# Optimization experiments

Measured on AMD Instinct MI355X. Metric: run time of the kernel, lower is better.

The kernel has to match this reference:

```python
import jax, jax.numpy as jnp
import numpy as np

LOG_STD_MAX = 2.0
LOG_STD_MIN = -5.0
LN_EPS = 1e-5


def layer_norm(x, scale, bias):
    mu = jnp.mean(x, axis=-1, keepdims=True)
    var = jnp.var(x, axis=-1, keepdims=True)
    return (x - mu) * jax.lax.rsqrt(var + LN_EPS) * scale + bias


def setup_inputs() -> dict:
    key = jax.random.key(0)
    B, OBS, ACT, H, M, K = 4096, 256, 32, 512, 16, 4
    ks = jax.random.split(key, 8)
    def w(k, shape, fan_in):
        return (jax.random.normal(k, shape, jnp.float32) / np.sqrt(fan_in)).astype(jnp.float32)
    return {
        "x": jax.random.normal(ks[0], (B, OBS), jnp.float32),
        "gate_W": w(ks[1], (OBS, M), OBS),
        "gate_b": jnp.zeros((M,), jnp.float32),
        "fc1_W": w(ks[2], (OBS, H * M), OBS),
        "fc1_b": jnp.zeros((H * M,), jnp.float32),
        "norm1_scale": jnp.ones((H * M,), jnp.float32),
        "norm1_bias": jnp.zeros((H * M,), jnp.float32),
        "fc2_W": w(ks[3], (H * M, H * M), H * M),
        "fc2_b": jnp.zeros((H * M,), jnp.float32),
        "norm2_scale": jnp.ones((H * M,), jnp.float32),
        "norm2_bias": jnp.zeros((H * M,), jnp.float32),
        "mean_W": w(ks[4], (H, ACT), H),
        "mean_b": jnp.zeros((ACT,), jnp.float32),
        "logstd_W": w(ks[5], (H, ACT), H),
        "logstd_b": jnp.zeros((ACT,), jnp.float32),
        "topk": K,
    }


def reference(x, gate_W, gate_b, fc1_W, fc1_b, norm1_scale, norm1_bias,
              fc2_W, fc2_b, norm2_scale, norm2_bias,
              mean_W, mean_b, logstd_W, logstd_b, topk):
    B = x.shape[0]
    M = gate_W.shape[1]
    # gating: softmax -> topk -> renormalize -> scatter into full [B, M] scores
    gate_scores = jax.nn.softmax(x @ gate_W + gate_b, axis=-1)  # [B, M]
    topk_vals, topk_idx = jax.lax.top_k(gate_scores, topk)       # [B, K]
    topk_vals = topk_vals / jnp.sum(topk_vals, axis=-1, keepdims=True)
    scores = jnp.zeros_like(gate_scores).at[jnp.arange(B)[:, None], topk_idx].set(topk_vals)
    # trunk: Linear -> LayerNorm -> ReLU, twice
    h = jax.nn.relu(layer_norm(x @ fc1_W + fc1_b, norm1_scale, norm1_bias))
    h = jax.nn.relu(layer_norm(h @ fc2_W + fc2_b, norm2_scale, norm2_bias))
    # reshape [B, H*M] -> [B, H, M] (expert m = strided slice), weighted MEAN over experts
    h = h.reshape(B, -1, M)                                      # [B, H, M]
    mixed = jnp.einsum('bhm,bm->bh', h, scores) / M              # mean, not sum
    mean = mixed @ mean_W + mean_b
    log_std = jnp.tanh(mixed @ logstd_W + logstd_b)
    log_std = LOG_STD_MIN + 0.5 * (LOG_STD_MAX - LOG_STD_MIN) * (log_std + 1.0)
    return mean, log_std
```

## Files before the change

kernel.cpp:

```cpp
#include <hip/hip_runtime.h>
#include <hip/hip_bf16.h>

typedef unsigned int u32;
typedef unsigned short u16;
typedef __bf16 bf16x8 __attribute__((ext_vector_type(8)));
typedef float f32x4 __attribute__((ext_vector_type(4)));

__device__ __forceinline__ u16 f2b(float f) {
    __bf16 b = (__bf16)f;
    return __builtin_bit_cast(u16, b);
}
__device__ __forceinline__ float b2f(u16 v) {
    u32 x = ((u32)v) << 16;
    return __builtin_bit_cast(float, x);
}

__device__ __forceinline__ void gld_lds16(const void* g, void* l) {
    __builtin_amdgcn_global_load_lds(
        (const __attribute__((address_space(1))) u32*)(size_t)g,
        (__attribute__((address_space(3))) u32*)(u32)(size_t)l,
        16, 0, 0);
}

#define BARRIER __builtin_amdgcn_s_barrier()
#define LGKM0 asm volatile("s_waitcnt lgkmcnt(0)" ::: "memory")
#define VMC4 asm volatile("s_waitcnt vmcnt(4)" ::: "memory")
#define VMC6 asm volatile("s_waitcnt vmcnt(6)" ::: "memory")
#define VMC0 asm volatile("s_waitcnt vmcnt(0)" ::: "memory")
#define MFMA16(d, a, b) d = __builtin_amdgcn_mfma_f32_16x16x32_bf16(a, b, d, 0, 0, 0)

__global__ __launch_bounds__(256) void cast_bf16_kernel(
    const float* __restrict__ in, u16* __restrict__ out, int n4)
{
    int i = blockIdx.x * 256 + threadIdx.x;
    if (i < n4) {
        float4 f = reinterpret_cast<const float4*>(in)[i];
        u32 lo = (u32)f2b(f.x) | ((u32)f2b(f.y) << 16);
        u32 hi = (u32)f2b(f.z) | ((u32)f2b(f.w) << 16);
        uint2 o; o.x = lo; o.y = hi;
        reinterpret_cast<uint2*>(out)[i] = o;
    }
}

__global__ __launch_bounds__(256) void transpose_cast_kernel(
    const float* __restrict__ in, u16* __restrict__ out, int R, int C)
{
    __shared__ float tile[64][65];
    const int t = threadIdx.x;
    const int c0 = blockIdx.x * 64;
    const int r0 = blockIdx.y * 64;
    #pragma unroll
    for (int i = 0; i < 4; ++i) {
        int idx = t + i * 256;
        int r = idx >> 4;
        int c = (idx & 15) * 4;
        float4 f = *reinterpret_cast<const float4*>(&in[(long)(r0 + r) * C + c0 + c]);
        tile[r][c] = f.x; tile[r][c + 1] = f.y; tile[r][c + 2] = f.z; tile[r][c + 3] = f.w;
    }
    __syncthreads();
    #pragma unroll
    for (int i = 0; i < 8; ++i) {
        int idx = t + i * 256;
        int rr = idx >> 5;
        int cc = idx & 31;
        u32 p = (u32)f2b(tile[cc * 2 + 0][rr]) | ((u32)f2b(tile[cc * 2 + 1][rr]) << 16);
        *reinterpret_cast<u32*>(&out[(long)(c0 + rr) * R + r0 + cc * 2]) = p;
    }
}

__global__ __launch_bounds__(256) void gate_kernel(
    const float* __restrict__ x, const float* __restrict__ gW,
    const float* __restrict__ gb, const int* __restrict__ topk,
    float* __restrict__ scores)
{
    const int t = threadIdx.x;
    const int row = blockIdx.x * 4 + (t >> 6);
    const int l = t & 63;
    const int m = l & 15;
    const int q = l >> 4;
    const int Kk = *topk;
    const float* xr = x + (long)row * 256;
    float p = 0.f;
    #pragma unroll
    for (int k4 = 0; k4 < 16; ++k4) {
        f32x4 xv = *reinterpret_cast<const f32x4*>(xr + q * 64 + k4 * 4);
        const int kb = q * 64 + k4 * 4;
        p += xv[0] * gW[(kb + 0) * 16 + m] + xv[1] * gW[(kb + 1) * 16 + m]
           + xv[2] * gW[(kb + 2) * 16 + m] + xv[3] * gW[(kb + 3) * 16 + m];
    }
    p += __shfl_xor(p, 16);
    p += __shfl_xor(p, 32);
    float logit = p + gb[m];
    float mx = logit;
    #pragma unroll
    for (int d = 1; d < 16; d <<= 1) mx = fmaxf(mx, __shfl_xor(mx, d));
    int rank = 0;
    #pragma unroll
    for (int j = 0; j < 16; ++j) {
        float vj = __shfl(logit, (l & 48) | j);
        rank += (vj > logit) || (vj == logit && j < m);
    }
    bool sel = rank < Kk;
    float e = sel ? expf(logit - mx) : 0.f;
    float ssum = e;
    #pragma unroll
    for (int d = 1; d < 16; d <<= 1) ssum += __shfl_xor(ssum, d);
    if (q == 0) scores[row * 16 + m] = e / ssum;
}


template<int GRAN>
__device__ __forceinline__ void stage_half(
    const u16* __restrict__ src, int ld, int rowbase, int kk,
    u16* ldsregion, int h, int w, int l)
{
    #pragma unroll
    for (int j = 0; j < 2; ++j) {
        const int c = w * 2 + j;
        const int o = c * 1024 + l * 16;
        const int os = o ^ (((o >> 7) & 7) << 4);
        const int pos = o >> 7;
        const int row = ((pos / GRAN) * 2 + h) * GRAN + (pos & (GRAN - 1));
        const u16* g = src + (long)(rowbase + row) * ld + kk + ((os & 127) >> 1);
        gld_lds16(g, ldsregion + c * 512);
    }
}

__device__ __forceinline__ bf16x8 ldfrag(const u16* region, int pos, int col) {
    const int o = (pos * 128 + col * 2) ^ ((pos & 7) << 4);
    return *reinterpret_cast<const bf16x8*>(reinterpret_cast<const char*>(region) + o);
}

template<int CB>
__device__ __forceinline__ void ktile_group(
    const u16* __restrict__ A, int lda, const u16* __restrict__ BT, int ldb,
    int brow, int bcol, int kkA1, int kkR,
    int wr, int wc, int r4, int q8, int w, int l,
    u16 (&lds)[2][4][8192], f32x4 (&acc)[8][4],
    bf16x8 (&bLu)[2][2], bf16x8 (&bLf)[2][2])
{
    bf16x8 aL[4][2], aH[4][2], bH[2][2];

    #pragma unroll
    for (int m = 0; m < 4; ++m) {
        aL[m][0] = ldfrag(lds[CB][0], wr * 64 + m * 16 + r4, q8);
        aL[m][1] = ldfrag(lds[CB][0], wr * 64 + m * 16 + r4, 32 + q8);
    }
    stage_half<64>(A, lda, brow, kkA1, &lds[1 - CB][1][0], 1, w, l);
    BARRIER; LGKM0;
    __builtin_amdgcn_s_setprio(1);
    #pragma unroll
    for (int m = 0; m < 4; ++m)
        #pragma unroll
        for (int n = 0; n < 2; ++n) {
            MFMA16(acc[m][n], aL[m][0], bLu[n][0]);
            MFMA16(acc[m][n], aL[m][1], bLu[n][1]);
        }
    __builtin_amdgcn_s_setprio(0);
    BARRIER;

    #pragma unroll
    for (int n = 0; n < 2; ++n) {
        bH[n][0] = ldfrag(lds[CB][3], wc * 32 + n * 16 + r4, q8);
        bH[n][1] = ldfrag(lds[CB][3], wc * 32 + n * 16 + r4, 32 + q8);
    }
    stage_half<64>(A, lda, brow, kkR, &lds[CB][0][0], 0, w, l);
    BARRIER; LGKM0;
    __builtin_amdgcn_s_setprio(1);
    #pragma unroll
    for (int m = 0; m < 4; ++m)
        #pragma unroll
        for (int n = 0; n < 2; ++n) {
            MFMA16(acc[m][2 + n], aL[m][0], bH[n][0]);
            MFMA16(acc[m][2 + n], aL[m][1], bH[n][1]);
        }
    __builtin_amdgcn_s_setprio(0);
    BARRIER;

    #pragma unroll
    for (int m = 0; m < 4; ++m) {
        aH[m][0] = ldfrag(lds[CB][1], wr * 64 + m * 16 + r4, q8);
        aH[m][1] = ldfrag(lds[CB][1], wr * 64 + m * 16 + r4, 32 + q8);
    }
    stage_half<32>(BT, ldb, bcol, kkR, &lds[CB][2][0], 0, w, l);
    BARRIER; LGKM0;
    __builtin_amdgcn_s_setprio(1);
    #pragma unroll
    for (int m = 0; m < 4; ++m)
        #pragma unroll
        for (int n = 0; n < 2; ++n) {
            MFMA16(acc[4 + m][2 + n], aH[m][0], bH[n][0]);
            MFMA16(acc[4 + m][2 + n], aH[m][1], bH[n][1]);
        }
    __builtin_amdgcn_s_setprio(0);
    VMC4;
    BARRIER;

    #pragma unroll
    for (int n = 0; n < 2; ++n) {
        bLf[n][0] = ldfrag(lds[1 - CB][2], wc * 32 + n * 16 + r4, q8);
        bLf[n][1] = ldfrag(lds[1 - CB][2], wc * 32 + n * 16 + r4, 32 + q8);
    }
    stage_half<32>(BT, ldb, bcol, kkR, &lds[CB][3][0], 1, w, l);
    BARRIER; LGKM0;
    __builtin_amdgcn_s_setprio(1);
    #pragma unroll
    for (int m = 0; m < 4; ++m)
        #pragma unroll
        for (int n = 0; n < 2; ++n) {
            MFMA16(acc[4 + m][n], aH[m][0], bLu[n][0]);
            MFMA16(acc[4 + m][n], aH[m][1], bLu[n][1]);
        }
    __builtin_amdgcn_s_setprio(0);
    BARRIER;
}

__global__ __launch_bounds__(512, 2) void gemm256(
    const u16* __restrict__ A, int lda,
    const u16* __restrict__ BT, int ldb,
    u16* __restrict__ C, int ldc, int K)
{
    __shared__ __align__(16) u16 lds[2][4][8192];
    const int t = threadIdx.x;
    const int w = t >> 6, l = t & 63;
    const int wr = w >> 2, wc = w & 3;
    const int r4 = l & 15, q8 = (l >> 4) * 8;
    const int bid = blockIdx.y * 32 + blockIdx.x;
    const int xcd = bid & 7, within = bid >> 3;
    const int by = (xcd >> 2) * 8 + (within >> 3);
    const int bx = (xcd & 3) * 8 + (within & 7);
    const int brow = by * 256, bcol = bx * 256;
    const int NT = K >> 6;

    f32x4 acc[8][4];
    #pragma unroll
    for (int m = 0; m < 8; ++m)
        #pragma unroll
        for (int n = 0; n < 4; ++n)
            acc[m][n] = (f32x4){0.f, 0.f, 0.f, 0.f};

    stage_half<64>(A, lda, brow, 0, &lds[0][0][0], 0, w, l);
    stage_half<32>(BT, ldb, bcol, 0, &lds[0][2][0], 0, w, l);
    stage_half<32>(BT, ldb, bcol, 0, &lds[0][3][0], 1, w, l);
    stage_half<64>(A, lda, brow, 0, &lds[0][1][0], 1, w, l);
    stage_half<64>(A, lda, brow, 64, &lds[1][0][0], 0, w, l);
    stage_half<32>(BT, ldb, bcol, 64, &lds[1][2][0], 0, w, l);
    stage_half<32>(BT, ldb, bcol, 64, &lds[1][3][0], 1, w, l);
    VMC6;
    BARRIER;

    bf16x8 bl0[2][2], bl1[2][2];
    #pragma unroll
    for (int n = 0; n < 2; ++n) {
        bl0[n][0] = ldfrag(lds[0][2], wc * 32 + n * 16 + r4, q8);
        bl0[n][1] = ldfrag(lds[0][2], wc * 32 + n * 16 + r4, 32 + q8);
    }

    for (int i = 0; i < (NT >> 1); ++i) {
        const int U = 2 * i;
        int tV = U + 1;
        int tU2 = U + 2;
        int tV2 = U + 3;
        if (tU2 >= NT) tU2 -= NT;
        if (tV2 >= NT) tV2 -= NT;
        const int kkV = (tV >= NT ? tV - NT : tV) << 6;
        const int kkU2 = tU2 << 6;
        const int kkV2 = tV2 << 6;

        ktile_group<0>(A, lda, BT, ldb, brow, bcol, kkV, kkU2,
                       wr, wc, r4, q8, w, l, lds, acc, bl0, bl1);
        ktile_group<1>(A, lda, BT, ldb, brow, bcol, kkU2, kkV2,
                       wr, wc, r4, q8, w, l, lds, acc, bl1, bl0);
    }

    VMC0;

    const int crow0 = (l >> 4) * 4;
    const int ccol = l & 15;
    #pragma unroll
    for (int m = 0; m < 8; ++m) {
        #pragma unroll
        for (int n = 0; n < 4; ++n) {
            int gr = brow + wr * 128 + m * 16 + crow0;
            int gc = bcol + wc * 64 + n * 16 + ccol;
            #pragma unroll
            for (int r = 0; r < 4; ++r)
                C[(long)(gr + r) * ldc + gc] = f2b(acc[m][n][r]);
        }
    }
}

__global__ __launch_bounds__(256) void ln1_kernel(
    const u16* __restrict__ Y, const float* __restrict__ fcb,
    const float* __restrict__ g, const float* __restrict__ be,
    u16* __restrict__ H)
{
    const int N = 8192;
    const int row = blockIdx.x;
    const int t = threadIdx.x;
    const u16* y = Y + (long)row * N;
    const int base = t * 32;
    float v[32];
    float s = 0.f, s2 = 0.f;
    #pragma unroll
    for (int j = 0; j < 4; ++j) {
        uint4 q = *reinterpret_cast<const uint4*>(y + base + j * 8);
        f32x4 cA = *reinterpret_cast<const f32x4*>(fcb + base + j * 8);
        f32x4 cB = *reinterpret_cast<const f32x4*>(fcb + base + j * 8 + 4);
        const u32 ww[4] = {q.x, q.y, q.z, q.w};
        const float cb[8] = {cA[0], cA[1], cA[2], cA[3], cB[0], cB[1], cB[2], cB[3]};
        #pragma unroll
        for (int e = 0; e < 4; ++e) {
            float a0 = b2f((u16)(ww[e] & 0xffff)) + cb[e * 2];
            float a1 = b2f((u16)(ww[e] >> 16)) + cb[e * 2 + 1];
            v[j * 8 + e * 2] = a0; v[j * 8 + e * 2 + 1] = a1;
            s += a0 + a1;
            s2 += a0 * a0 + a1 * a1;
        }
    }
    #pragma unroll
    for (int d = 32; d > 0; d >>= 1) { s += __shfl_down(s, d); s2 += __shfl_down(s2, d); }
    __shared__ float red[8];
    if ((t & 63) == 0) { red[t >> 6] = s; red[4 + (t >> 6)] = s2; }
    __syncthreads();
    s = red[0] + red[1] + red[2] + red[3];
    s2 = red[4] + red[5] + red[6] + red[7];
    float mu = s * (1.f / N);
    float var = s2 * (1.f / N) - mu * mu;
    float rs = rsqrtf(var + 1e-5f);
    __align__(16) u16 o[32];
    #pragma unroll
    for (int j = 0; j < 4; ++j) {
        f32x4 gA = *reinterpret_cast<const f32x4*>(g + base + j * 8);
        f32x4 gB = *reinterpret_cast<const f32x4*>(g + base + j * 8 + 4);
        f32x4 eA = *reinterpret_cast<const f32x4*>(be + base + j * 8);
        f32x4 eB = *reinterpret_cast<const f32x4*>(be + base + j * 8 + 4);
        const float gg[8] = {gA[0], gA[1], gA[2], gA[3], gB[0], gB[1], gB[2], gB[3]};
        const float ee[8] = {eA[0], eA[1], eA[2], eA[3], eB[0], eB[1], eB[2], eB[3]};
        #pragma unroll
        for (int k = 0; k < 8; ++k) {
            float z = (v[j * 8 + k] - mu) * rs * gg[k] + ee[k];
            o[j * 8 + k] = f2b(fmaxf(z, 0.f));
        }
    }
    u16* h = H + (long)row * N + base;
    #pragma unroll
    for (int j = 0; j < 4; ++j)
        *reinterpret_cast<uint4*>(h + j * 8) = *reinterpret_cast<const uint4*>(&o[j * 8]);
}

__global__ __launch_bounds__(256) void ln2_mix_kernel(
    const u16* __restrict__ Y, const float* __restrict__ fcb,
    const float* __restrict__ g, const float* __restrict__ be,
    const float* __restrict__ scores, float* __restrict__ mixed)
{
    const int N = 8192;
    const int row = blockIdx.x;
    const int t = threadIdx.x;
    const u16* y = Y + (long)row * N;
    const int base = t * 32;
    __shared__ float sc[16];
    if (t < 16) sc[t] = scores[row * 16 + t];
    float v[32];
    float s = 0.f, s2 = 0.f;
    #pragma unroll
    for (int j = 0; j < 4; ++j) {
        uint4 q = *reinterpret_cast<const uint4*>(y + base + j * 8);
        f32x4 cA = *reinterpret_cast<const f32x4*>(fcb + base + j * 8);
        f32x4 cB = *reinterpret_cast<const f32x4*>(fcb + base + j * 8 + 4);
        const u32 ww[4] = {q.x, q.y, q.z, q.w};
        const float cb[8] = {cA[0], cA[1], cA[2], cA[3], cB[0], cB[1], cB[2], cB[3]};
        #pragma unroll
        for (int e = 0; e < 4; ++e) {
            float a0 = b2f((u16)(ww[e] & 0xffff)) + cb[e * 2];
            float a1 = b2f((u16)(ww[e] >> 16)) + cb[e * 2 + 1];
            v[j * 8 + e * 2] = a0; v[j * 8 + e * 2 + 1] = a1;
            s += a0 + a1;
            s2 += a0 * a0 + a1 * a1;
        }
    }
    #pragma unroll
    for (int d = 32; d > 0; d >>= 1) { s += __shfl_down(s, d); s2 += __shfl_down(s2, d); }
    __shared__ float red[8];
    if ((t & 63) == 0) { red[t >> 6] = s; red[4 + (t >> 6)] = s2; }
    __syncthreads();
    s = red[0] + red[1] + red[2] + red[3];
    s2 = red[4] + red[5] + red[6] + red[7];
    float mu = s * (1.f / N);
    float var = s2 * (1.f / N) - mu * mu;
    float rs = rsqrtf(var + 1e-5f);
    float m0 = 0.f, m1 = 0.f;
    #pragma unroll
    for (int j = 0; j < 4; ++j) {
        f32x4 g0 = *reinterpret_cast<const f32x4*>(g + base + j * 4);
        f32x4 e0 = *reinterpret_cast<const f32x4*>(be + base + j * 4);
        f32x4 g1 = *reinterpret_cast<const f32x4*>(g + base + 16 + j * 4);
        f32x4 e1 = *reinterpret_cast<const f32x4*>(be + base + 16 + j * 4);
        #pragma unroll
        for (int k = 0; k < 4; ++k) {
            int m = j * 4 + k;
            float z0 = fmaxf((v[m] - mu) * rs * g0[k] + e0[k], 0.f);
            float z1 = fmaxf((v[16 + m] - mu) * rs * g1[k] + e1[k], 0.f);
            m0 += z0 * sc[m];
            m1 += z1 * sc[m];
        }
    }
    float2 outv; outv.x = m0 * (1.f / 16.f); outv.y = m1 * (1.f / 16.f);
    *reinterpret_cast<float2*>(&mixed[(long)row * 512 + 2 * t]) = outv;
}

__global__ __launch_bounds__(256) void heads_kernel(
    const float* __restrict__ mixed, const float* __restrict__ mW,
    const float* __restrict__ mb, const float* __restrict__ sW,
    const float* __restrict__ sb, float* __restrict__ out)
{
    const int B = 4096;
    __shared__ float wm[512 * 32];
    __shared__ float wsd[512 * 32];
    __shared__ float mx[8][512];
    const int t = threadIdx.x;
    const int rb = blockIdx.x * 8;
    for (int i = t; i < 4096; i += 256) {
        reinterpret_cast<float4*>(wm)[i]  = reinterpret_cast<const float4*>(mW)[i];
        reinterpret_cast<float4*>(wsd)[i] = reinterpret_cast<const float4*>(sW)[i];
    }
    for (int i = t; i < 1024; i += 256) {
        reinterpret_cast<float4*>(&mx[0][0])[i] =
            reinterpret_cast<const float4*>(mixed + (long)rb * 512)[i];
    }
    __syncthreads();
    const int bl = t >> 5;
    const int a = t & 31;
    float am = mb[a], as = sb[a];
    #pragma unroll 4
    for (int h = 0; h < 512; ++h) {
        float xv = mx[bl][h];
        am += xv * wm[h * 32 + a];
        as += xv * wsd[h * 32 + a];
    }
    int row = rb + bl;
    out[(long)row * 32 + a] = am;
    float ts = tanhf(as);
    out[(long)B * 32 + (long)row * 32 + a] = -5.0f + 3.5f * (ts + 1.0f);
}

extern "C" void kernel_launch(void* const* d_in, const int* in_sizes, int n_in,
                              void* d_out, int out_size, void* d_ws, size_t ws_size,
                              hipStream_t stream) {
    const float* x   = (const float*)d_in[0];
    const float* gW  = (const float*)d_in[1];
    const float* gb  = (const float*)d_in[2];
    const float* w1  = (const float*)d_in[3];
    const float* b1  = (const float*)d_in[4];
    const float* g1  = (const float*)d_in[5];
    const float* be1 = (const float*)d_in[6];
    const float* w2  = (const float*)d_in[7];
    const float* b2  = (const float*)d_in[8];
    const float* g2  = (const float*)d_in[9];
    const float* be2 = (const float*)d_in[10];
    const float* mW  = (const float*)d_in[11];
    const float* mb  = (const float*)d_in[12];
    const float* sW  = (const float*)d_in[13];
    const float* sb  = (const float*)d_in[14];
    const int* topk  = (const int*)d_in[15];
    float* out = (float*)d_out;

    char* ws = (char*)d_ws;
    u16* W2T = (u16*)ws;            ws += (long)8192 * 8192 * 2;
    u16* Yb = (u16*)ws;             ws += (long)4096 * 8192 * 2;
    u16* H1 = (u16*)ws;             ws += (long)4096 * 8192 * 2;
    u16* W1T = (u16*)ws;            ws += (long)8192 * 256 * 2;
    u16* XB = (u16*)ws;             ws += (long)4096 * 256 * 2;
    float* SCR = (float*)ws;        ws += (long)4096 * 16 * 4;
    float* MIX = (float*)ws;        ws += (long)4096 * 512 * 4;

    cast_bf16_kernel<<<1024, 256, 0, stream>>>(x, XB, 262144);
    transpose_cast_kernel<<<dim3(128, 4), 256, 0, stream>>>(w1, W1T, 256, 8192);
    transpose_cast_kernel<<<dim3(128, 128), 256, 0, stream>>>(w2, W2T, 8192, 8192);
    gate_kernel<<<1024, 256, 0, stream>>>(x, gW, gb, topk, SCR);

    gemm256<<<dim3(32, 16), 512, 0, stream>>>(XB, 256, W1T, 256, Yb, 8192, 256);
    ln1_kernel<<<4096, 256, 0, stream>>>(Yb, b1, g1, be1, H1);

    gemm256<<<dim3(32, 16), 512, 0, stream>>>(H1, 8192, W2T, 8192, Yb, 8192, 8192);
    ln2_mix_kernel<<<4096, 256, 0, stream>>>(Yb, b2, g2, be2, SCR, MIX);

    heads_kernel<<<512, 256, 0, stream>>>(MIX, mW, mb, sW, sb, out);
}
```

Before: 724.6 us.

## Fuse small kernels and drop a barrier in GEMM inner stage

Merges the x cast with the gate kernel, merges both weight transposes into one launch, and folds the output heads into the LN2/mix kernel so the mixed activations never go to global memory. Also moves the final B staging ahead of the fragment loads and removes a barrier plus LDS wait in the GEMM main loop. This cuts launch overhead and one intermediate buffer. The dropped barrier risks a race between the LDS fragment reads and the asynchronous staging writes, and the fused heads re-read the head weights from global memory in every row block.

```diff
diff --git a/kernel.cpp b/kernel.cpp
--- a/kernel.cpp
+++ b/kernel.cpp
@@ -29,51 +29,20 @@
 #define VMC0 asm volatile("s_waitcnt vmcnt(0)" ::: "memory")
 #define MFMA16(d, a, b) d = __builtin_amdgcn_mfma_f32_16x16x32_bf16(a, b, d, 0, 0, 0)
 
-__global__ __launch_bounds__(256) void cast_bf16_kernel(
-    const float* __restrict__ in, u16* __restrict__ out, int n4)
-{
-    int i = blockIdx.x * 256 + threadIdx.x;
-    if (i < n4) {
-        float4 f = reinterpret_cast<const float4*>(in)[i];
+__global__ __launch_bounds__(256) void castgate_kernel(
+    const float* __restrict__ x, const float* __restrict__ gW,
+    const float* __restrict__ gb, const int* __restrict__ topk,
+    u16* __restrict__ XB, float* __restrict__ scores)
+{
+    const int t = threadIdx.x;
+    {
+        int i = blockIdx.x * 256 + t;
+        float4 f = reinterpret_cast<const float4*>(x)[i];
         u32 lo = (u32)f2b(f.x) | ((u32)f2b(f.y) << 16);
         u32 hi = (u32)f2b(f.z) | ((u32)f2b(f.w) << 16);
         uint2 o; o.x = lo; o.y = hi;
-        reinterpret_cast<uint2*>(out)[i] = o;
-    }
-}
-
-__global__ __launch_bounds__(256) void transpose_cast_kernel(
-    const float* __restrict__ in, u16* __restrict__ out, int R, int C)
-{
-    __shared__ float tile[64][65];
-    const int t = threadIdx.x;
-    const int c0 = blockIdx.x * 64;
-    const int r0 = blockIdx.y * 64;
-    #pragma unroll
-    for (int i = 0; i < 4; ++i) {
-        int idx = t + i * 256;
-        int r = idx >> 4;
-        int c = (idx & 15) * 4;
-        float4 f = *reinterpret_cast<const float4*>(&in[(long)(r0 + r) * C + c0 + c]);
-        tile[r][c] = f.x; tile[r][c + 1] = f.y; tile[r][c + 2] = f.z; tile[r][c + 3] = f.w;
-    }
-    __syncthreads();
-    #pragma unroll
-    for (int i = 0; i < 8; ++i) {
-        int idx = t + i * 256;
-        int rr = idx >> 5;
-        int cc = idx & 31;
-        u32 p = (u32)f2b(tile[cc * 2 + 0][rr]) | ((u32)f2b(tile[cc * 2 + 1][rr]) << 16);
-        *reinterpret_cast<u32*>(&out[(long)(c0 + rr) * R + r0 + cc * 2]) = p;
-    }
-}
-
-__global__ __launch_bounds__(256) void gate_kernel(
-    const float* __restrict__ x, const float* __restrict__ gW,
-    const float* __restrict__ gb, const int* __restrict__ topk,
-    float* __restrict__ scores)
-{
-    const int t = threadIdx.x;
+        reinterpret_cast<uint2*>(XB)[i] = o;
+    }
     const int row = blockIdx.x * 4 + (t >> 6);
     const int l = t & 63;
     const int m = l & 15;
@@ -106,6 +75,39 @@
     #pragma unroll
     for (int d = 1; d < 16; d <<= 1) ssum += __shfl_xor(ssum, d);
     if (q == 0) scores[row * 16 + m] = e / ssum;
+}
+
+__global__ __launch_bounds__(256) void transpose_both_kernel(
+    const float* __restrict__ w2, u16* __restrict__ W2T,
+    const float* __restrict__ w1, u16* __restrict__ W1T)
+{
+    __shared__ float tile[64][65];
+    const int t = threadIdx.x;
+    const int byy = blockIdx.y;
+    const float* in;
+    u16* outp;
+    int R, r0;
+    if (byy < 128) { in = w2; outp = W2T; R = 8192; r0 = byy * 64; }
+    else           { in = w1; outp = W1T; R = 256;  r0 = (byy - 128) * 64; }
+    const int C = 8192;
+    const int c0 = blockIdx.x * 64;
+    #pragma unroll
+    for (int i = 0; i < 4; ++i) {
+        int idx = t + i * 256;
+        int r = idx >> 4;
+        int c = (idx & 15) * 4;
+        float4 f = *reinterpret_cast<const float4*>(&in[(long)(r0 + r) * C + c0 + c]);
+        tile[r][c] = f.x; tile[r][c + 1] = f.y; tile[r][c + 2] = f.z; tile[r][c + 3] = f.w;
+    }
+    __syncthreads();
+    #pragma unroll
+    for (int i = 0; i < 8; ++i) {
+        int idx = t + i * 256;
+        int rr = idx >> 5;
+        int cc = idx & 31;
+        u32 p = (u32)f2b(tile[cc * 2 + 0][rr]) | ((u32)f2b(tile[cc * 2 + 1][rr]) << 16);
+        *reinterpret_cast<u32*>(&outp[(long)(c0 + rr) * R + r0 + cc * 2]) = p;
+    }
 }
 
 
@@ -196,13 +198,12 @@
     VMC4;
     BARRIER;
 
+    stage_half<32>(BT, ldb, bcol, kkR, &lds[CB][3][0], 1, w, l);
     #pragma unroll
     for (int n = 0; n < 2; ++n) {
         bLf[n][0] = ldfrag(lds[1 - CB][2], wc * 32 + n * 16 + r4, q8);
         bLf[n][1] = ldfrag(lds[1 - CB][2], wc * 32 + n * 16 + r4, 32 + q8);
     }
-    stage_half<32>(BT, ldb, bcol, kkR, &lds[CB][3][0], 1, w, l);
-    BARRIER; LGKM0;
     __builtin_amdgcn_s_setprio(1);
     #pragma unroll
     for (int m = 0; m < 4; ++m)
@@ -349,12 +350,16 @@
         *reinterpret_cast<uint4*>(h + j * 8) = *reinterpret_cast<const uint4*>(&o[j * 8]);
 }
 
-__global__ __launch_bounds__(256) void ln2_mix_kernel(
+__global__ __launch_bounds__(256) void ln2_mix_heads_kernel(
     const u16* __restrict__ Y, const float* __restrict__ fcb,
     const float* __restrict__ g, const float* __restrict__ be,
-    const float* __restrict__ scores, float* __restrict__ mixed)
+    const float* __restrict__ scores,
+    const float* __restrict__ mW, const float* __restrict__ mb,
+    const float* __restrict__ sW, const float* __restrict__ sb,
+    float* __restrict__ out)
 {
     const int N = 8192;
+    const int B = 4096;
     const int row = blockIdx.x;
     const int t = threadIdx.x;
     const u16* y = Y + (long)row * N;
@@ -405,43 +410,37 @@
             m1 += z1 * sc[m];
         }
     }
-    float2 outv; outv.x = m0 * (1.f / 16.f); outv.y = m1 * (1.f / 16.f);
-    *reinterpret_cast<float2*>(&mixed[(long)row * 512 + 2 * t]) = outv;
-}
-
-__global__ __launch_bounds__(256) void heads_kernel(
-    const float* __restrict__ mixed, const float* __restrict__ mW,
-    const float* __restrict__ mb, const float* __restrict__ sW,
-    const float* __restrict__ sb, float* __restrict__ out)
-{
-    const int B = 4096;
-    __shared__ float wm[512 * 32];
-    __shared__ float wsd[512 * 32];
-    __shared__ float mx[8][512];
-    const int t = threadIdx.x;
-    const int rb = blockIdx.x * 8;
-    for (int i = t; i < 4096; i += 256) {
-        reinterpret_cast<float4*>(wm)[i]  = reinterpret_cast<const float4*>(mW)[i];
-        reinterpret_cast<float4*>(wsd)[i] = reinterpret_cast<const float4*>(sW)[i];
-    }
-    for (int i = t; i < 1024; i += 256) {
-        reinterpret_cast<float4*>(&mx[0][0])[i] =
-            reinterpret_cast<const float4*>(mixed + (long)rb * 512)[i];
-    }
+    __shared__ float mix[512];
+    mix[2 * t]     = m0 * (1.f / 16.f);
+    mix[2 * t + 1] = m1 * (1.f / 16.f);
     __syncthreads();
-    const int bl = t >> 5;
     const int a = t & 31;
-    float am = mb[a], as = sb[a];
+    const int seg = t >> 5;
+    float pm = 0.f, ps = 0.f;
     #pragma unroll 4
-    for (int h = 0; h < 512; ++h) {
-        float xv = mx[bl][h];
-        am += xv * wm[h * 32 + a];
-        as += xv * wsd[h * 32 + a];
-    }
-    int row = rb + bl;
-    out[(long)row * 32 + a] = am;
-    float ts = tanhf(as);
-    out[(long)B * 32 + (long)row * 32 + a] = -5.0f + 3.5f * (ts + 1.0f);
+    for (int h = seg * 64; h < seg * 64 + 64; ++h) {
+        float xv = mix[h];
+        pm += xv * mW[h * 32 + a];
+        ps += xv * sW[h * 32 + a];
+    }
+    __shared__ float prm[8][32];
+    __shared__ float prs[8][32];
+    prm[seg][a] = pm;
+    prs[seg][a] = ps;
+    __syncthreads();
+    if (t < 32) {
+        float am = mb[t];
+        #pragma unroll
+        for (int ss = 0; ss < 8; ++ss) am += prm[ss][t];
+        out[(long)row * 32 + t] = am;
+    } else if (t < 64) {
+        int aa = t - 32;
+        float as = sb[aa];
+        #pragma unroll
+        for (int ss = 0; ss < 8; ++ss) as += prs[ss][aa];
+        float ts = tanhf(as);
+        out[(long)B * 32 + (long)row * 32 + aa] = -5.0f + 3.5f * (ts + 1.0f);
+    }
 }
 
 extern "C" void kernel_launch(void* const* d_in, const int* in_sizes, int n_in,
@@ -472,18 +471,14 @@
     u16* W1T = (u16*)ws;            ws += (long)8192 * 256 * 2;
     u16* XB = (u16*)ws;             ws += (long)4096 * 256 * 2;
     float* SCR = (float*)ws;        ws += (long)4096 * 16 * 4;
-    float* MIX = (float*)ws;        ws += (long)4096 * 512 * 4;
-
-    cast_bf16_kernel<<<1024, 256, 0, stream>>>(x, XB, 262144);
-    transpose_cast_kernel<<<dim3(128, 4), 256, 0, stream>>>(w1, W1T, 256, 8192);
-    transpose_cast_kernel<<<dim3(128, 128), 256, 0, stream>>>(w2, W2T, 8192, 8192);
-    gate_kernel<<<1024, 256, 0, stream>>>(x, gW, gb, topk, SCR);
+
+    castgate_kernel<<<1024, 256, 0, stream>>>(x, gW, gb, topk, XB, SCR);
+    transpose_both_kernel<<<dim3(128, 132), 256, 0, stream>>>(w2, W2T, w1, W1T);
 
     gemm256<<<dim3(32, 16), 512, 0, stream>>>(XB, 256, W1T, 256, Yb, 8192, 256);
     ln1_kernel<<<4096, 256, 0, stream>>>(Yb, b1, g1, be1, H1);
 
     gemm256<<<dim3(32, 16), 512, 0, stream>>>(H1, 8192, W2T, 8192, Yb, 8192, 8192);
-    ln2_mix_kernel<<<4096, 256, 0, stream>>>(Yb, b2, g2, be2, SCR, MIX);
-
-    heads_kernel<<<512, 256, 0, stream>>>(MIX, mW, mb, sW, sb, out);
-}
+    ln2_mix_heads_kernel<<<4096, 256, 0, stream>>>(Yb, b2, g2, be2, SCR,
+                                                   mW, mb, sW, sb, out);
+}
```

New measurement: 706.0 us. 2.6% less time.
